# Optimization experiments

Measured on AMD Instinct MI355X. Metric: run time of the kernel, lower is better.

## Reference

```python
import jax, jax.numpy as jnp
import numpy as np

N = 50000
HID = 128
NH = 4
E_RES, E_SEQ, E_KNN = 100000, 100000, 200000
BN_EPS = 1e-5
NEG_SLOPE = 0.2


def _gat(h, src, dst, W, al, ar, resW, b):
    """DGL-style GATConv (eval mode: feat_drop off, residual=True, bias).
    h: (N, in), W/resW: (in, H*out), al/ar: (H, out), b: (H*out,)"""
    Hh, out = al.shape
    feat = (h @ W).reshape(N, Hh, out)                 # (N, H, out)
    el = jnp.sum(feat * al, axis=-1)                   # (N, H)
    er = jnp.sum(feat * ar, axis=-1)                   # (N, H)
    e = jax.nn.leaky_relu(el[src] + er[dst], NEG_SLOPE)  # (E, H)
    # edge softmax over incoming edges of each dst node (numerically stable)
    m = jax.ops.segment_max(e, dst, num_segments=N)    # (N, H)
    ex = jnp.exp(e - m[dst])
    s = jax.ops.segment_sum(ex, dst, num_segments=N)
    a = ex / s[dst]                                    # (E, H)
    msg = a[:, :, None] * feat[src]                    # (E, H, out)
    rst = jax.ops.segment_sum(msg, dst, num_segments=N)  # (N, H, out)
    return rst + (h @ resW).reshape(N, Hh, out) + b.reshape(1, Hh, out)


def _hetero(h, src_res, dst_res, src_seq, dst_seq, src_knn, dst_knn, W, al, ar, resW, b):
    # HeteroGraphConv with aggregate='sum' over relations, then mean over heads
    r = _gat(h, src_res, dst_res, W[0], al[0], ar[0], resW[0], b[0])
    r = r + _gat(h, src_seq, dst_seq, W[1], al[1], ar[1], resW[1], b[1])
    r = r + _gat(h, src_knn, dst_knn, W[2], al[2], ar[2], resW[2], b[2])
    return jnp.mean(r, axis=1)                         # (N, out)


def setup_inputs() -> dict:
    key = jax.random.key(0)
    ks = iter(jax.random.split(key, 32))
    inp = {}
    inp["x"] = jax.random.normal(next(ks), (N, HID), jnp.float32)
    inp["src_res"] = jax.random.randint(next(ks), (E_RES,), 0, N, jnp.int32)
    inp["dst_res"] = jax.random.randint(next(ks), (E_RES,), 0, N, jnp.int32)
    inp["src_seq"] = jax.random.randint(next(ks), (E_SEQ,), 0, N, jnp.int32)
    inp["dst_seq"] = jax.random.randint(next(ks), (E_SEQ,), 0, N, jnp.int32)
    inp["src_knn"] = jax.random.randint(next(ks), (E_KNN,), 0, N, jnp.int32)
    inp["dst_knn"] = jax.random.randint(next(ks), (E_KNN,), 0, N, jnp.int32)
    sc = 0.05
    for l in (0, 1):
        inp[f"W{l}"] = jax.random.normal(next(ks), (3, HID, NH * HID), jnp.float32) * sc
        inp[f"al{l}"] = jax.random.normal(next(ks), (3, NH, HID), jnp.float32) * sc
        inp[f"ar{l}"] = jax.random.normal(next(ks), (3, NH, HID), jnp.float32) * sc
        inp[f"resW{l}"] = jax.random.normal(next(ks), (3, HID, NH * HID), jnp.float32) * sc
        inp[f"b{l}"] = jax.random.normal(next(ks), (3, NH * HID), jnp.float32) * sc
    inp["fc_W"] = jax.random.normal(next(ks), (HID, HID), jnp.float32) * sc
    inp["fc_b"] = jax.random.normal(next(ks), (HID,), jnp.float32) * sc
    inp["bn_gamma"] = jnp.ones((HID,), jnp.float32)
    inp["bn_beta"] = jnp.zeros((HID,), jnp.float32)
    inp["bn_mean"] = jax.random.normal(next(ks), (HID,), jnp.float32) * sc
    inp["bn_var"] = jax.random.uniform(next(ks), (HID,), jnp.float32)
    return inp


def reference(x, src_res, dst_res, src_seq, dst_seq, src_knn, dst_knn,
              W0, al0, ar0, resW0, b0, W1, al1, ar1, resW1, b1,
              fc_W, fc_b, bn_gamma, bn_beta, bn_mean, bn_var):
    # layer 0: hetero GAT, head-mean, fc + ReLU + BatchNorm (eval), dropout=identity
    h = _hetero(x, src_res, dst_res, src_seq, dst_seq, src_knn, dst_knn,
                W0, al0, ar0, resW0, b0)
    h = jax.nn.relu(h @ fc_W + fc_b)
    h = (h - bn_mean) / jnp.sqrt(bn_var + BN_EPS) * bn_gamma + bn_beta
    # layer 1 (final): hetero GAT, head-mean
    out = _hetero(h, src_res, dst_res, src_seq, dst_seq, src_knn, dst_knn,
                  W1, al1, ar1, resW1, b1)
    return out
```

## Files before the change

kernel.cpp:

```cpp
#include <hip/hip_runtime.h>
#include <hip/hip_bf16.h>
#include <math.h>
#include <stdint.h>

#define NNODES 50000
#define SCHUNK 4096
#define AW 1664
#define XOFF 1536

typedef __bf16 bf16x8 __attribute__((ext_vector_type(8)));
typedef float f32x4 __attribute__((ext_vector_type(4)));
typedef unsigned short u16;
typedef unsigned int u32;

__device__ __forceinline__ float lrelu(float x){ return x >= 0.f ? x : 0.2f*x; }
__device__ __forceinline__ float b2f(u16 u){ union{ u32 i; float f; } c; c.i = ((u32)u)<<16; return c.f; }
__device__ __forceinline__ float lo2f(u32 v){ union{ u32 i; float f; } c; c.i = v<<16; return c.f; }
__device__ __forceinline__ float hi2f(u32 v){ union{ u32 i; float f; } c; c.i = v & 0xffff0000u; return c.f; }
__device__ __forceinline__ u16 f2b(float f){ __hip_bfloat16 h = __float2bfloat16(f); return *(u16*)&h; }
__device__ __forceinline__ u32 packbf(float a, float b){ return (u32)f2b(a) | ((u32)f2b(b) << 16); }

#define GLDS16(g, l) __builtin_amdgcn_global_load_lds( \
    (const __attribute__((address_space(1))) void*)(g), \
    (__attribute__((address_space(3))) void*)(l), 16, 0, 0)

__global__ void prep_b(const float* __restrict__ W0, const float* __restrict__ W1,
                       const float* __restrict__ resW0, const float* __restrict__ resW1,
                       const float* __restrict__ b0, const float* __restrict__ b1,
                       u16* __restrict__ Btb, float* __restrict__ biasf)
{
    int gid = blockIdx.x*blockDim.x + threadIdx.x;
    if (gid < 2*128*AW){
        int l = gid / (128*AW);
        int rem = gid - l*(128*AW);
        int c = rem / AW;
        int j = rem - c*AW;
        const float* W  = l ? W1 : W0;
        const float* rw = l ? resW1 : resW0;
        float v;
        if (j < XOFF){
            int r = j >> 9, h = (j >> 7) & 3, k = j & 127;
            v = 0.25f * W[(size_t)r*65536 + (size_t)k*512 + h*128 + c];
        } else {
            int k = j - XOFF;
            float s = 0.f;
            for (int r = 0; r < 3; ++r)
                for (int h = 0; h < 4; ++h)
                    s += rw[(size_t)r*65536 + (size_t)k*512 + h*128 + c];
            v = 0.25f * s;
        }
        Btb[gid] = f2b(v);
    }
    if (gid < 256){
        int l = gid >> 7, c = gid & 127;
        const float* bb = l ? b1 : b0;
        float s = 0.f;
        for (int r = 0; r < 3; ++r)
            for (int h = 0; h < 4; ++h)
                s += bb[r*512 + h*128 + c];
        biasf[gid] = 0.25f*s;
    }
}

__global__ void prep_wl(const float* __restrict__ W0, const float* __restrict__ W1,
                        const float* __restrict__ al0, const float* __restrict__ ar0,
                        const float* __restrict__ al1, const float* __restrict__ ar1,
                        const float* __restrict__ fcW,
                        u16* __restrict__ wlb, u16* __restrict__ fcWtb)
{
    int gid = blockIdx.x*blockDim.x + threadIdx.x;
    if (gid < 2*128*128){
        int l = gid >> 14;
        int col = (gid >> 7) & 127;
        int k = gid & 127;
        float v = 0.f;
        if (col < 24){
            int r = col >> 3, lr = (col >> 2) & 1, h = col & 3;
            const float* W = l ? W1 : W0;
            const float* av = l ? (lr ? ar1 : al1) : (lr ? ar0 : al0);
            const float* wrow = W + (size_t)r*65536 + (size_t)k*512 + h*128;
            const float* arow = av + r*512 + h*128;
            for (int cc = 0; cc < 128; ++cc) v += wrow[cc]*arow[cc];
        }
        wlb[gid] = f2b(v);
    }
    if (gid < 128*128){
        int k = gid & 127, n = gid >> 7;
        fcWtb[gid] = f2b(fcW[k*128 + n]);
    }
}

__global__ __launch_bounds__(256) void xprep_kernel(const float* __restrict__ x,
    u16* __restrict__ Ax, const u16* __restrict__ wl, float* __restrict__ el, int M)
{
    __shared__ u16 Xs[64*136];
    __shared__ u16 Ws[32*136];
    const int tid = threadIdx.x;
    const int row0 = blockIdx.x*64;
    #pragma unroll
    for (int p = 0; p < 2; ++p){
        int idx = tid + p*256;
        int c = idx >> 4, kc = (idx & 15)*8;
        float4 v = make_float4(0.f,0.f,0.f,0.f);
        if (c < 24) v = *(const float4*)(wl + c*128 + kc);
        *(float4*)&Ws[c*136 + kc] = v;
    }
    int r = tid >> 2, cq = (tid & 3)*32;
    int grow = row0 + r;
    if (grow < M){
        #pragma unroll
        for (int i = 0; i < 8; ++i){
            float4 v = *(const float4*)(x + (size_t)grow*128 + cq + i*4);
            ushort4 o;
            o.x = f2b(v.x); o.y = f2b(v.y); o.z = f2b(v.z); o.w = f2b(v.w);
            *(ushort4*)(Ax + (size_t)grow*AW + cq + i*4) = o;
            *(ushort4*)&Xs[r*136 + cq + i*4] = o;
        }
    } else {
        ushort4 z; z.x=0; z.y=0; z.z=0; z.w=0;
        #pragma unroll
        for (int i = 0; i < 8; ++i) *(ushort4*)&Xs[r*136 + cq + i*4] = z;
    }
    __syncthreads();
    const int lane = tid & 63, wave = tid >> 6;
    const int r16 = lane & 15, quad = lane >> 4;
    f32x4 acc0 = {}, acc1 = {};
    #pragma unroll
    for (int ks = 0; ks < 4; ++ks){
        int ko = ks*32 + quad*8;
        bf16x8 a  = *(const bf16x8*)&Xs[(wave*16 + r16)*136 + ko];
        bf16x8 b0 = *(const bf16x8*)&Ws[r16*136 + ko];
        bf16x8 b1 = *(const bf16x8*)&Ws[(16 + r16)*136 + ko];
        acc0 = __builtin_amdgcn_mfma_f32_16x16x32_bf16(a, b0, acc0, 0,0,0);
        acc1 = __builtin_amdgcn_mfma_f32_16x16x32_bf16(a, b1, acc1, 0,0,0);
    }
    #pragma unroll
    for (int p = 0; p < 4; ++p){
        int row = row0 + wave*16 + quad*4 + p;
        if (row < M){
            el[(size_t)row*32 + r16] = acc0[p];
            if (r16 < 8) el[(size_t)row*32 + 16 + r16] = acc1[p];
        }
    }
}

__global__ void hist_all(const int* __restrict__ d0, const int* __restrict__ d1,
                         const int* __restrict__ d2, int e0, int e1, int e2,
                         int* __restrict__ cnt)
{
    int g = blockIdx.x*blockDim.x + threadIdx.x;
    if (g >= e0 + e1 + e2) return;
    int rel, idx;
    if (g < e0){ rel = 0; idx = g; }
    else if (g < e0 + e1){ rel = 1; idx = g - e0; }
    else { rel = 2; idx = g - e0 - e1; }
    const int* d = rel == 0 ? d0 : (rel == 1 ? d1 : d2);
    atomicAdd(cnt + (size_t)rel*NNODES + d[idx], 1);
}

__global__ __launch_bounds__(256) void scan_part(const int* __restrict__ cnt_all,
                                                 int* __restrict__ partials, int Nn, int nblk)
{
    int rel = blockIdx.y, blk = blockIdx.x;
    const int* cnt = cnt_all + (size_t)rel*Nn;
    int tid = threadIdx.x;
    int i0 = blk*SCHUNK + tid*16;
    int s = 0;
    #pragma unroll
    for (int k = 0; k < 4; ++k){
        int idx = i0 + k*4;
        if (idx + 3 < Nn){ int4 v = *(const int4*)(cnt + idx); s += v.x+v.y+v.z+v.w; }
        else { for (int j = 0; j < 4; ++j) if (idx+j < Nn) s += cnt[idx+j]; }
    }
    #pragma unroll
    for (int off = 1; off < 64; off <<= 1) s += __shfl_xor(s, off);
    __shared__ int ws[4];
    if ((tid & 63) == 0) ws[tid>>6] = s;
    __syncthreads();
    if (tid == 0) partials[rel*nblk + blk] = ws[0]+ws[1]+ws[2]+ws[3];
}

__global__ __launch_bounds__(256) void scan_write(const int* __restrict__ cnt_all,
                                                  const int* __restrict__ partials,
                                                  int* __restrict__ rp_all, int* __restrict__ cur_all,
                                                  int Nn, int nblk)
{
    int rel = blockIdx.y, blk = blockIdx.x;
    const int* cnt = cnt_all + (size_t)rel*Nn;
    int* rp  = rp_all  + (size_t)rel*(Nn+1);
    int* cur = cur_all + (size_t)rel*Nn;
    int tid = threadIdx.x;
    __shared__ int sOff;
    __shared__ int wsum[4];
    if (tid == 0){
        int o = 0;
        for (int b = 0; b < blk; ++b) o += partials[rel*nblk + b];
        sOff = o;
        if (blk == 0){
            int t = 0;
            for (int b = 0; b < nblk; ++b) t += partials[rel*nblk + b];
            rp[Nn] = t;
        }
    }
    int i0 = blk*SCHUNK + tid*16;
    int v[16];
    int s = 0;
    #pragma unroll
    for (int k = 0; k < 16; ++k){
        int idx = i0 + k;
        v[k] = (idx < Nn) ? cnt[idx] : 0;
        s += v[k];
    }
    int lane = tid & 63;
    int incl = s;
    #pragma unroll
    for (int off = 1; off < 64; off <<= 1){
        int t = __shfl_up(incl, off);
        if (lane >= off) incl += t;
    }
    if (lane == 63) wsum[tid>>6] = incl;
    __syncthreads();
    int woff = 0;
    for (int w = 0; w < (tid>>6); ++w) woff += wsum[w];
    int ex = sOff + woff + incl - s;
    #pragma unroll
    for (int k = 0; k < 16; ++k){
        int idx = i0 + k;
        if (idx < Nn){ rp[idx] = ex; cur[idx] = ex; }
        ex += v[k];
    }
}

__global__ void scatter_all(const int* __restrict__ s0, const int* __restrict__ s1,
                            const int* __restrict__ s2,
                            const int* __restrict__ d0, const int* __restrict__ d1,
                            const int* __restrict__ d2, int e0, int e1, int e2,
                            int* __restrict__ cur, int* __restrict__ colb,
                            int* __restrict__ dste)
{
    int g = blockIdx.x*blockDim.x + threadIdx.x;
    if (g >= e0 + e1 + e2) return;
    int rel, idx, coff;
    if (g < e0){ rel = 0; idx = g; coff = 0; }
    else if (g < e0 + e1){ rel = 1; idx = g - e0; coff = e0; }
    else { rel = 2; idx = g - e0 - e1; coff = e0 + e1; }
    const int* sp = rel == 0 ? s0 : (rel == 1 ? s1 : s2);
    const int* dp = rel == 0 ? d0 : (rel == 1 ? d1 : d2);
    int d = dp[idx];
    int pos = atomicAdd(cur + (size_t)rel*NNODES + d, 1);
    colb[coff + pos] = sp[idx];
    dste[coff + pos] = d;
}

__global__ void wprep(const int* __restrict__ colb, const int* __restrict__ dste,
                      int e0, int e01, int etot,
                      const float* __restrict__ el_all, uint4* __restrict__ rec)
{
    int j = blockIdx.x*blockDim.x + threadIdx.x;
    if (j >= etot) return;
    int rel = (j < e0) ? 0 : ((j < e01) ? 1 : 2);
    int src = colb[j], dst = dste[j];
    float4 es = *(const float4*)(el_all + (size_t)src*32 + rel*8);
    float4 ed = *(const float4*)(el_all + (size_t)dst*32 + rel*8 + 4);
    uint4 o;
    o.x = (u32)src;
    o.y = packbf(__expf(lrelu(es.x + ed.x)), __expf(lrelu(es.y + ed.y)));
    o.z = packbf(__expf(lrelu(es.z + ed.z)), __expf(lrelu(es.w + ed.w)));
    o.w = 0;
    rec[j] = o;
}

__global__ __launch_bounds__(256) void agg3(const int* __restrict__ rowp_all,
    const uint4* __restrict__ rec_all, int e0, int e01,
    const u16* __restrict__ Ax, u16* __restrict__ Abuf, int Nn)
{
    const int rel = blockIdx.y;
    const int tid = threadIdx.x;
    const int o = tid & 15;
    const int n = (blockIdx.x*256 + tid) >> 4;
    if (n >= Nn) return;
    const int* rowp = rowp_all + (size_t)rel*(Nn+1);
    const int coff = (rel == 0) ? 0 : ((rel == 1) ? e0 : e01);
    const uint4* rec = rec_all + coff;
    u16* op = Abuf + (size_t)n*AW + rel*512 + o*8;

    int beg = rowp[n], end = rowp[n+1];
    if (beg >= end){
        uint4 z; z.x = 0; z.y = 0; z.z = 0; z.w = 0;
        #pragma unroll
        for (int h = 0; h < 4; ++h) *(uint4*)(op + h*128) = z;
        return;
    }
    float acc[4][8] = {};
    float us0 = 0.f, us1 = 0.f, us2 = 0.f, us3 = 0.f;

    uint4 ra = rec[beg];
    uint4 xa = *(const uint4*)(Ax + (size_t)ra.x*AW + o*8);
    uint4 rb = ra, xb = xa;
    if (beg + 1 < end){
        rb = rec[beg+1];
        xb = *(const uint4*)(Ax + (size_t)rb.x*AW + o*8);
    }
    for (int j = beg; j < end; ++j){
        uint4 rc = rb, xc = xb;
        if (j + 2 < end){
            rc = rec[j+2];
            xc = *(const uint4*)(Ax + (size_t)rc.x*AW + o*8);
        }
        float w0 = lo2f(ra.y), w1 = hi2f(ra.y), w2 = lo2f(ra.z), w3 = hi2f(ra.z);
        us0 += w0; us1 += w1; us2 += w2; us3 += w3;
        float xv[8];
        xv[0] = lo2f(xa.x); xv[1] = hi2f(xa.x);
        xv[2] = lo2f(xa.y); xv[3] = hi2f(xa.y);
        xv[4] = lo2f(xa.z); xv[5] = hi2f(xa.z);
        xv[6] = lo2f(xa.w); xv[7] = hi2f(xa.w);
        #pragma unroll
        for (int c = 0; c < 8; ++c){
            acc[0][c] = fmaf(w0, xv[c], acc[0][c]);
            acc[1][c] = fmaf(w1, xv[c], acc[1][c]);
            acc[2][c] = fmaf(w2, xv[c], acc[2][c]);
            acc[3][c] = fmaf(w3, xv[c], acc[3][c]);
        }
        ra = rb; xa = xb; rb = rc; xb = xc;
    }
    float inv[4] = {1.f/us0, 1.f/us1, 1.f/us2, 1.f/us3};
    #pragma unroll
    for (int h = 0; h < 4; ++h){
        uint4 ov;
        ov.x = packbf(acc[h][0]*inv[h], acc[h][1]*inv[h]);
        ov.y = packbf(acc[h][2]*inv[h], acc[h][3]*inv[h]);
        ov.z = packbf(acc[h][4]*inv[h], acc[h][5]*inv[h]);
        ov.w = packbf(acc[h][6]*inv[h], acc[h][7]*inv[h]);
        *(uint4*)(op + h*128) = ov;
    }
}

template<int EPI, int ELR>
__global__ __launch_bounds__(256) void gemm_f(
    const u16* __restrict__ A, int Astride, int K,
    const u16* __restrict__ Bt,
    float* __restrict__ Cf, u16* __restrict__ Cb, int Cstride, int M,
    const float* __restrict__ bias, const float* __restrict__ gamma,
    const float* __restrict__ beta, const float* __restrict__ mean,
    const float* __restrict__ var,
    const u16* __restrict__ wl, float* __restrict__ el)
{
    __shared__ u16 smem[24576];
    const int tid = threadIdx.x;
    const int row0 = blockIdx.x*64;
    const int lane = tid & 63, wave = tid >> 6;
    const int wm = (wave >> 1)*32, wn = (wave & 1)*64;
    const int r16 = lane & 15, quad = lane >> 4;
    const int swzbase = r16 & 7;
    f32x4 acc[2][4] = {};

    const int r8 = lane >> 3, jc = lane & 7;
    const int soff = ((jc ^ r8) << 3);
    int gA0 = row0 + wave*16 + r8;      if (gA0 >= M) gA0 = M - 1;
    int gA1 = row0 + wave*16 + 8 + r8;  if (gA1 >= M) gA1 = M - 1;
    const u16* srcA0 = A + (size_t)gA0*Astride + soff;
    const u16* srcA1 = A + (size_t)gA1*Astride + soff;
    const u16* srcB0 = Bt + (size_t)(wave*32      + r8)*K + soff;
    const u16* srcB1 = Bt + (size_t)(wave*32 + 8  + r8)*K + soff;
    const u16* srcB2 = Bt + (size_t)(wave*32 + 16 + r8)*K + soff;
    const u16* srcB3 = Bt + (size_t)(wave*32 + 24 + r8)*K + soff;
    const int nk = K >> 6;

    #define STAGE(buf, k0) do { \
        u16* As_ = smem + (buf)*12288; \
        u16* Bs_ = As_ + 4096; \
        GLDS16(srcA0 + (k0), As_ + wave*1024); \
        GLDS16(srcA1 + (k0), As_ + wave*1024 + 512); \
        GLDS16(srcB0 + (k0), Bs_ + wave*2048); \
        GLDS16(srcB1 + (k0), Bs_ + wave*2048 + 512); \
        GLDS16(srcB2 + (k0), Bs_ + wave*2048 + 1024); \
        GLDS16(srcB3 + (k0), Bs_ + wave*2048 + 1536); \
    } while (0)

    STAGE(0, 0);
    __syncthreads();
    for (int t = 0; t < nk; ++t){
        int cur = t & 1;
        if (t + 1 < nk) STAGE(cur ^ 1, (t + 1) << 6);
        const u16* As = smem + cur*12288;
        const u16* Bs = As + 4096;
        #pragma unroll
        for (int ks = 0; ks < 2; ++ks){
            int swz = ((ks*4 + quad) ^ swzbase) << 3;
            bf16x8 a0 = *(const bf16x8*)&As[(wm + r16)*64 + swz];
            bf16x8 a1 = *(const bf16x8*)&As[(wm + 16 + r16)*64 + swz];
            #pragma unroll
            for (int j = 0; j < 4; ++j){
                bf16x8 b = *(const bf16x8*)&Bs[(wn + j*16 + r16)*64 + swz];
                acc[0][j] = __builtin_amdgcn_mfma_f32_16x16x32_bf16(a0, b, acc[0][j], 0,0,0);
                acc[1][j] = __builtin_amdgcn_mfma_f32_16x16x32_bf16(a1, b, acc[1][j], 0,0,0);
            }
        }
        __syncthreads();
    }
    #undef STAGE

    u16* Cs = smem;
    u16* Ws = smem + 64*136;
    if (ELR){
        #pragma unroll
        for (int p = 0; p < 2; ++p){
            int idx = tid + p*256;
            int c = idx >> 4, kc = (idx & 15)*8;
            float4 v = make_float4(0.f,0.f,0.f,0.f);
            if (c < 24) v = *(const float4*)(wl + c*128 + kc);
            *(float4*)&Ws[c*136 + kc] = v;
        }
    }
    #pragma unroll
    for (int i = 0; i < 2; ++i){
        #pragma unroll
        for (int p = 0; p < 4; ++p){
            int rl = wm + i*16 + quad*4 + p;
            int row = row0 + rl;
            #pragma unroll
            for (int j = 0; j < 4; ++j){
                int col = wn + j*16 + r16;
                float v = acc[i][j][p] + bias[col];
                if (EPI == 2){
                    float t = fmaxf(v, 0.f);
                    v = (t - mean[col]) * rsqrtf(var[col] + 1e-5f) * gamma[col] + beta[col];
                }
                u16 vb = f2b(v);
                if (row < M){
                    if (EPI == 1) Cf[(size_t)row*Cstride + col] = v;
                    else          Cb[(size_t)row*Cstride + col] = vb;
                }
                if (ELR) Cs[rl*136 + col] = vb;
            }
        }
    }
    if (ELR){
        __syncthreads();
        f32x4 e0 = {}, e1 = {};
        #pragma unroll
        for (int ks = 0; ks < 4; ++ks){
            int ko = ks*32 + quad*8;
            bf16x8 a  = *(const bf16x8*)&Cs[(wave*16 + r16)*136 + ko];
            bf16x8 b0 = *(const bf16x8*)&Ws[r16*136 + ko];
            bf16x8 b1 = *(const bf16x8*)&Ws[(16 + r16)*136 + ko];
            e0 = __builtin_amdgcn_mfma_f32_16x16x32_bf16(a, b0, e0, 0,0,0);
            e1 = __builtin_amdgcn_mfma_f32_16x16x32_bf16(a, b1, e1, 0,0,0);
        }
        #pragma unroll
        for (int p = 0; p < 4; ++p){
            int row = row0 + wave*16 + quad*4 + p;
            if (row < M){
                el[(size_t)row*32 + r16] = e0[p];
                if (r16 < 8) el[(size_t)row*32 + 16 + r16] = e1[p];
            }
        }
    }
}

static inline char* align256(char* p){ return (char*)(((uintptr_t)p + 255) & ~(uintptr_t)255); }

extern "C" void kernel_launch(void* const* d_in, const int* in_sizes, int n_in,
                              void* d_out, int out_size, void* d_ws, size_t ws_size,
                              hipStream_t stream)
{
    const float* x      = (const float*)d_in[0];
    const int* srcs[3]  = {(const int*)d_in[1], (const int*)d_in[3], (const int*)d_in[5]};
    const int* dsts[3]  = {(const int*)d_in[2], (const int*)d_in[4], (const int*)d_in[6]};
    const int  E[3]     = {in_sizes[1], in_sizes[3], in_sizes[5]};
    const float* W0     = (const float*)d_in[7];
    const float* al0    = (const float*)d_in[8];
    const float* ar0    = (const float*)d_in[9];
    const float* resW0  = (const float*)d_in[10];
    const float* b0     = (const float*)d_in[11];
    const float* W1     = (const float*)d_in[12];
    const float* al1    = (const float*)d_in[13];
    const float* ar1    = (const float*)d_in[14];
    const float* resW1  = (const float*)d_in[15];
    const float* b1     = (const float*)d_in[16];
    const float* fcW    = (const float*)d_in[17];
    const float* fcb    = (const float*)d_in[18];
    const float* gamma  = (const float*)d_in[19];
    const float* beta   = (const float*)d_in[20];
    const float* bmean  = (const float*)d_in[21];
    const float* bvar   = (const float*)d_in[22];
    float* out = (float*)d_out;

    char* p = (char*)d_ws;
    u16*   Abuf  = (u16*)p;   p += (size_t)NNODES*AW*2;    p = align256(p);
    float* el    = (float*)p; p += (size_t)NNODES*32*4;    p = align256(p);
    u16*   hmb   = (u16*)p;   p += (size_t)NNODES*128*2;   p = align256(p);
    int*   cnt   = (int*)p;   p += (size_t)3*NNODES*4;     p = align256(p);
    int*   rowp  = (int*)p;   p += (size_t)3*(NNODES+1)*4; p = align256(p);
    int*   cur   = (int*)p;   p += (size_t)3*NNODES*4;     p = align256(p);
    int*   colb  = (int*)p;   p += (size_t)(E[0]+E[1]+E[2])*4; p = align256(p);
    int*   dste  = (int*)p;   p += (size_t)(E[0]+E[1]+E[2])*4; p = align256(p);
    uint4* rec   = (uint4*)p; p += (size_t)(E[0]+E[1]+E[2])*16; p = align256(p);
    u16*   Btb   = (u16*)p;   p += (size_t)2*128*AW*2;     p = align256(p);
    u16*   wlb   = (u16*)p;   p += (size_t)2*128*128*2;    p = align256(p);
    u16*   fcWtb = (u16*)p;   p += (size_t)128*128*2;      p = align256(p);
    float* biasf = (float*)p; p += (size_t)2*128*4;        p = align256(p);
    int*   parts = (int*)p;   p += (size_t)3*64*4;

    const int NBLK = (NNODES + SCHUNK - 1)/SCHUNK;
    const int MB = (NNODES + 63)/64;
    const int AGGBLKS = (NNODES*16 + 255)/256;
    const int ETOT = E[0] + E[1] + E[2];
    dim3 blk(256);
    u16* Ax = Abuf + XOFF;

    hipMemsetAsync(cnt, 0, (size_t)3*NNODES*sizeof(int), stream);
    prep_b <<<(2*128*AW + 255)/256, blk, 0, stream>>>(W0, W1, resW0, resW1, b0, b1, Btb, biasf);
    prep_wl<<<(2*128*128 + 255)/256, blk, 0, stream>>>(W0, W1, al0, ar0, al1, ar1, fcW, wlb, fcWtb);
    xprep_kernel<<<MB, blk, 0, stream>>>(x, Ax, wlb, el, NNODES);
    hist_all<<<(ETOT + 255)/256, blk, 0, stream>>>(dsts[0], dsts[1], dsts[2], E[0], E[1], E[2], cnt);
    scan_part <<<dim3(NBLK,3), blk, 0, stream>>>(cnt, parts, NNODES, NBLK);
    scan_write<<<dim3(NBLK,3), blk, 0, stream>>>(cnt, parts, rowp, cur, NNODES, NBLK);
    scatter_all<<<(ETOT + 255)/256, blk, 0, stream>>>(srcs[0], srcs[1], srcs[2],
                                                      dsts[0], dsts[1], dsts[2],
                                                      E[0], E[1], E[2], cur, colb, dste);

    wprep<<<(ETOT + 255)/256, blk, 0, stream>>>(colb, dste, E[0], E[0]+E[1], ETOT, el, rec);
    agg3<<<dim3(AGGBLKS,3), blk, 0, stream>>>(rowp, rec, E[0], E[0]+E[1], Ax, Abuf, NNODES);
    gemm_f<4,0><<<MB, blk, 0, stream>>>(Abuf, AW, AW, Btb, nullptr, hmb, 128, NNODES,
                                        biasf, nullptr, nullptr, nullptr, nullptr, nullptr, nullptr);
    gemm_f<2,1><<<MB, blk, 0, stream>>>(hmb, 128, 128, fcWtb, nullptr, Ax, AW, NNODES,
                                        fcb, gamma, beta, bmean, bvar, wlb + 16384, el);

    wprep<<<(ETOT + 255)/256, blk, 0, stream>>>(colb, dste, E[0], E[0]+E[1], ETOT, el, rec);
    agg3<<<dim3(AGGBLKS,3), blk, 0, stream>>>(rowp, rec, E[0], E[0]+E[1], Ax, Abuf, NNODES);
    gemm_f<1,0><<<MB, blk, 0, stream>>>(Abuf, AW, AW, Btb + (size_t)128*AW, out, nullptr, 128, NNODES,
                                        biasf + 128, nullptr, nullptr, nullptr, nullptr, nullptr, nullptr);
}
```

Before: 390.0 us.

## Fuse edge aggregation with projection GEMM to drop wide intermediate buffer

Replaces the separate aggregation kernel and the wide 1664-column GEMM with one fused kernel. Each wave aggregates neighbor features for 16 rows per relation in registers, packs them directly into MFMA A-fragments, and multiplies against B tiles streamed into LDS with double buffering. The residual term comes from a compact 128-wide X buffer. This removes the write and re-read of the large Abuf intermediate. In exchange it uses heavy register pressure (128 floats of accumulators plus 16 fragments), per-block syncs, and serialises edge aggregation with the MFMA work, giving lower gather parallelism (one lane group per row instead of 16 threads per row per relation).

```diff
diff --git a/kernel.cpp b/kernel.cpp
--- a/kernel.cpp
+++ b/kernel.cpp
@@ -14,7 +14,6 @@
 typedef unsigned int u32;
 
 __device__ __forceinline__ float lrelu(float x){ return x >= 0.f ? x : 0.2f*x; }
-__device__ __forceinline__ float b2f(u16 u){ union{ u32 i; float f; } c; c.i = ((u32)u)<<16; return c.f; }
 __device__ __forceinline__ float lo2f(u32 v){ union{ u32 i; float f; } c; c.i = v<<16; return c.f; }
 __device__ __forceinline__ float hi2f(u32 v){ union{ u32 i; float f; } c; c.i = v & 0xffff0000u; return c.f; }
 __device__ __forceinline__ u16 f2b(float f){ __hip_bfloat16 h = __float2bfloat16(f); return *(u16*)&h; }
@@ -49,7 +48,7 @@
                     s += rw[(size_t)r*65536 + (size_t)k*512 + h*128 + c];
             v = 0.25f * s;
         }
-        Btb[gid] = f2b(v);
+        Btb[(size_t)l*128*AW + (size_t)(j>>3)*1024 + c*8 + (j&7)] = f2b(v);
     }
     if (gid < 256){
         int l = gid >> 7, c = gid & 127;
@@ -91,7 +90,7 @@
 }
 
 __global__ __launch_bounds__(256) void xprep_kernel(const float* __restrict__ x,
-    u16* __restrict__ Ax, const u16* __restrict__ wl, float* __restrict__ el, int M)
+    u16* __restrict__ Xg, const u16* __restrict__ wl, float* __restrict__ el, int M)
 {
     __shared__ u16 Xs[64*136];
     __shared__ u16 Ws[32*136];
@@ -113,7 +112,7 @@
             float4 v = *(const float4*)(x + (size_t)grow*128 + cq + i*4);
             ushort4 o;
             o.x = f2b(v.x); o.y = f2b(v.y); o.z = f2b(v.z); o.w = f2b(v.w);
-            *(ushort4*)(Ax + (size_t)grow*AW + cq + i*4) = o;
+            *(ushort4*)(Xg + (size_t)grow*128 + cq + i*4) = o;
             *(ushort4*)&Xs[r*136 + cq + i*4] = o;
         }
     } else {
@@ -270,68 +269,138 @@
     rec[j] = o;
 }
 
-__global__ __launch_bounds__(256) void agg3(const int* __restrict__ rowp_all,
-    const uint4* __restrict__ rec_all, int e0, int e01,
-    const u16* __restrict__ Ax, u16* __restrict__ Abuf, int Nn)
-{
-    const int rel = blockIdx.y;
+template<int EPI>
+__global__ __launch_bounds__(256, 2) void fused_gat(
+    const int* __restrict__ rowp_all, const uint4* __restrict__ rec_all,
+    int e0, int e01,
+    const u16* __restrict__ Xg, const u16* __restrict__ Btg,
+    float* __restrict__ Cf, u16* __restrict__ Cb, int M,
+    const float* __restrict__ bias)
+{
+    __shared__ u16 smem[8192];
     const int tid = threadIdx.x;
-    const int o = tid & 15;
-    const int n = (blockIdx.x*256 + tid) >> 4;
-    if (n >= Nn) return;
-    const int* rowp = rowp_all + (size_t)rel*(Nn+1);
-    const int coff = (rel == 0) ? 0 : ((rel == 1) ? e0 : e01);
-    const uint4* rec = rec_all + coff;
-    u16* op = Abuf + (size_t)n*AW + rel*512 + o*8;
-
-    int beg = rowp[n], end = rowp[n+1];
-    if (beg >= end){
-        uint4 z; z.x = 0; z.y = 0; z.z = 0; z.w = 0;
-        #pragma unroll
-        for (int h = 0; h < 4; ++h) *(uint4*)(op + h*128) = z;
-        return;
-    }
-    float acc[4][8] = {};
-    float us0 = 0.f, us1 = 0.f, us2 = 0.f, us3 = 0.f;
-
-    uint4 ra = rec[beg];
-    uint4 xa = *(const uint4*)(Ax + (size_t)ra.x*AW + o*8);
-    uint4 rb = ra, xb = xa;
-    if (beg + 1 < end){
-        rb = rec[beg+1];
-        xb = *(const uint4*)(Ax + (size_t)rb.x*AW + o*8);
-    }
-    for (int j = beg; j < end; ++j){
-        uint4 rc = rb, xc = xb;
-        if (j + 2 < end){
-            rc = rec[j+2];
-            xc = *(const uint4*)(Ax + (size_t)rc.x*AW + o*8);
-        }
-        float w0 = lo2f(ra.y), w1 = hi2f(ra.y), w2 = lo2f(ra.z), w3 = hi2f(ra.z);
-        us0 += w0; us1 += w1; us2 += w2; us3 += w3;
-        float xv[8];
-        xv[0] = lo2f(xa.x); xv[1] = hi2f(xa.x);
-        xv[2] = lo2f(xa.y); xv[3] = hi2f(xa.y);
-        xv[4] = lo2f(xa.z); xv[5] = hi2f(xa.z);
-        xv[6] = lo2f(xa.w); xv[7] = hi2f(xa.w);
-        #pragma unroll
-        for (int c = 0; c < 8; ++c){
-            acc[0][c] = fmaf(w0, xv[c], acc[0][c]);
-            acc[1][c] = fmaf(w1, xv[c], acc[1][c]);
-            acc[2][c] = fmaf(w2, xv[c], acc[2][c]);
-            acc[3][c] = fmaf(w3, xv[c], acc[3][c]);
-        }
-        ra = rb; xa = xb; rb = rc; xb = xc;
-    }
-    float inv[4] = {1.f/us0, 1.f/us1, 1.f/us2, 1.f/us3};
-    #pragma unroll
-    for (int h = 0; h < 4; ++h){
-        uint4 ov;
-        ov.x = packbf(acc[h][0]*inv[h], acc[h][1]*inv[h]);
-        ov.y = packbf(acc[h][2]*inv[h], acc[h][3]*inv[h]);
-        ov.z = packbf(acc[h][4]*inv[h], acc[h][5]*inv[h]);
-        ov.w = packbf(acc[h][6]*inv[h], acc[h][7]*inv[h]);
-        *(uint4*)(op + h*128) = ov;
+    const int lane = tid & 63, wave = tid >> 6;
+    const int r16 = lane & 15, quad = lane >> 4;
+    const int row0 = blockIdx.x*64;
+    const int nd = row0 + wave*16 + r16;
+
+    f32x4 cacc[8] = {};
+    bf16x8 afrag[16];
+
+    #define STAGEB(buf, t) do { \
+        const u16* s0_ = Btg + (size_t)(t)*4096; \
+        GLDS16(s0_ + tid*8,        smem + (buf)*4096 + wave*512); \
+        GLDS16(s0_ + 2048 + tid*8, smem + (buf)*4096 + 2048 + wave*512); \
+    } while(0)
+
+    STAGEB(0, 0);
+
+    for (int r = 0; r < 3; ++r){
+        const int* rp = rowp_all + (size_t)r*(NNODES+1);
+        int beg = 0, end = 0;
+        if (nd < M){ beg = rp[nd]; end = rp[nd+1]; }
+        const int coff = (r == 0) ? 0 : ((r == 1) ? e0 : e01);
+        const uint4* rc = rec_all + coff;
+        float ac[4][4][8] = {};
+        float us0 = 0.f, us1 = 0.f, us2 = 0.f, us3 = 0.f;
+        uint4 ra = {0,0,0,0};
+        uint4 p0 = {0,0,0,0}, p1 = {0,0,0,0}, p2 = {0,0,0,0}, p3 = {0,0,0,0};
+        if (beg < end){
+            ra = rc[beg];
+            const u16* xr = Xg + (size_t)ra.x*128 + quad*8;
+            p0 = *(const uint4*)(xr);      p1 = *(const uint4*)(xr + 32);
+            p2 = *(const uint4*)(xr + 64); p3 = *(const uint4*)(xr + 96);
+        }
+        for (int j = beg; j < end; ++j){
+            uint4 rb = ra, q0 = p0, q1 = p1, q2 = p2, q3 = p3;
+            if (j + 1 < end){
+                rb = rc[j+1];
+                const u16* xr = Xg + (size_t)rb.x*128 + quad*8;
+                q0 = *(const uint4*)(xr);      q1 = *(const uint4*)(xr + 32);
+                q2 = *(const uint4*)(xr + 64); q3 = *(const uint4*)(xr + 96);
+            }
+            float w0 = lo2f(ra.y), w1 = hi2f(ra.y), w2 = lo2f(ra.z), w3 = hi2f(ra.z);
+            us0 += w0; us1 += w1; us2 += w2; us3 += w3;
+            #define PROCM(m, pv) do { \
+                float xv[8]; \
+                xv[0]=lo2f(pv.x); xv[1]=hi2f(pv.x); xv[2]=lo2f(pv.y); xv[3]=hi2f(pv.y); \
+                xv[4]=lo2f(pv.z); xv[5]=hi2f(pv.z); xv[6]=lo2f(pv.w); xv[7]=hi2f(pv.w); \
+                _Pragma("unroll") \
+                for (int c = 0; c < 8; ++c){ \
+                    ac[0][m][c] = fmaf(w0, xv[c], ac[0][m][c]); \
+                    ac[1][m][c] = fmaf(w1, xv[c], ac[1][m][c]); \
+                    ac[2][m][c] = fmaf(w2, xv[c], ac[2][m][c]); \
+                    ac[3][m][c] = fmaf(w3, xv[c], ac[3][m][c]); \
+                } \
+            } while(0)
+            PROCM(0, p0); PROCM(1, p1); PROCM(2, p2); PROCM(3, p3);
+            #undef PROCM
+            ra = rb; p0 = q0; p1 = q1; p2 = q2; p3 = q3;
+        }
+        float ivs[4];
+        ivs[0] = us0 > 0.f ? 1.f/us0 : 0.f;
+        ivs[1] = us1 > 0.f ? 1.f/us1 : 0.f;
+        ivs[2] = us2 > 0.f ? 1.f/us2 : 0.f;
+        ivs[3] = us3 > 0.f ? 1.f/us3 : 0.f;
+        #pragma unroll
+        for (int h = 0; h < 4; ++h){
+            #pragma unroll
+            for (int m = 0; m < 4; ++m){
+                union { bf16x8 v; u32 w[4]; } u;
+                u.w[0] = packbf(ac[h][m][0]*ivs[h], ac[h][m][1]*ivs[h]);
+                u.w[1] = packbf(ac[h][m][2]*ivs[h], ac[h][m][3]*ivs[h]);
+                u.w[2] = packbf(ac[h][m][4]*ivs[h], ac[h][m][5]*ivs[h]);
+                u.w[3] = packbf(ac[h][m][6]*ivs[h], ac[h][m][7]*ivs[h]);
+                afrag[h*4 + m] = u.v;
+            }
+        }
+        if (r == 0) __syncthreads();
+        #pragma unroll
+        for (int m2 = 0; m2 < 16; ++m2){
+            STAGEB((m2+1)&1, r*16 + m2 + 1);
+            const u16* Bs = smem + (m2&1)*4096 + quad*1024;
+            #pragma unroll
+            for (int j = 0; j < 8; ++j){
+                bf16x8 b = *(const bf16x8*)&Bs[(j*16 + r16)*8];
+                cacc[j] = __builtin_amdgcn_mfma_f32_16x16x32_bf16(afrag[m2], b, cacc[j], 0,0,0);
+            }
+            __syncthreads();
+        }
+    }
+    {
+        int xrow = nd < M ? nd : M - 1;
+        const u16* xr = Xg + (size_t)xrow*128 + quad*8;
+        bf16x8 xf0 = *(const bf16x8*)(xr);
+        bf16x8 xf1 = *(const bf16x8*)(xr + 32);
+        bf16x8 xf2 = *(const bf16x8*)(xr + 64);
+        bf16x8 xf3 = *(const bf16x8*)(xr + 96);
+        #pragma unroll
+        for (int m2 = 0; m2 < 4; ++m2){
+            if (m2 < 3) STAGEB((m2+1)&1, 49 + m2);
+            const u16* Bs = smem + (m2&1)*4096 + quad*1024;
+            bf16x8 a = m2 == 0 ? xf0 : (m2 == 1 ? xf1 : (m2 == 2 ? xf2 : xf3));
+            #pragma unroll
+            for (int j = 0; j < 8; ++j){
+                bf16x8 b = *(const bf16x8*)&Bs[(j*16 + r16)*8];
+                cacc[j] = __builtin_amdgcn_mfma_f32_16x16x32_bf16(a, b, cacc[j], 0,0,0);
+            }
+            __syncthreads();
+        }
+    }
+    #undef STAGEB
+    #pragma unroll
+    for (int j = 0; j < 8; ++j){
+        int col = j*16 + r16;
+        float bi = bias[col];
+        #pragma unroll
+        for (int p = 0; p < 4; ++p){
+            int row = row0 + wave*16 + quad*4 + p;
+            if (row < M){
+                float v = cacc[j][p] + bi;
+                if (EPI == 1) Cf[(size_t)row*128 + col] = v;
+                else          Cb[(size_t)row*128 + col] = f2b(v);
+            }
+        }
     }
 }
 
@@ -487,9 +556,10 @@
     float* out = (float*)d_out;
 
     char* p = (char*)d_ws;
-    u16*   Abuf  = (u16*)p;   p += (size_t)NNODES*AW*2;    p = align256(p);
+    u16*   Xg    = (u16*)p;   p += (size_t)NNODES*128*2;   p = align256(p);
+    u16*   hx1   = (u16*)p;   p += (size_t)NNODES*128*2;   p = align256(p);
+    u16*   hmb   = (u16*)p;   p += (size_t)NNODES*128*2;   p = align256(p);
     float* el    = (float*)p; p += (size_t)NNODES*32*4;    p = align256(p);
-    u16*   hmb   = (u16*)p;   p += (size_t)NNODES*128*2;   p = align256(p);
     int*   cnt   = (int*)p;   p += (size_t)3*NNODES*4;     p = align256(p);
     int*   rowp  = (int*)p;   p += (size_t)3*(NNODES+1)*4; p = align256(p);
     int*   cur   = (int*)p;   p += (size_t)3*NNODES*4;     p = align256(p);
@@ -504,15 +574,13 @@
 
     const int NBLK = (NNODES + SCHUNK - 1)/SCHUNK;
     const int MB = (NNODES + 63)/64;
-    const int AGGBLKS = (NNODES*16 + 255)/256;
     const int ETOT = E[0] + E[1] + E[2];
     dim3 blk(256);
-    u16* Ax = Abuf + XOFF;
 
     hipMemsetAsync(cnt, 0, (size_t)3*NNODES*sizeof(int), stream);
     prep_b <<<(2*128*AW + 255)/256, blk, 0, stream>>>(W0, W1, resW0, resW1, b0, b1, Btb, biasf);
     prep_wl<<<(2*128*128 + 255)/256, blk, 0, stream>>>(W0, W1, al0, ar0, al1, ar1, fcW, wlb, fcWtb);
-    xprep_kernel<<<MB, blk, 0, stream>>>(x, Ax, wlb, el, NNODES);
+    xprep_kernel<<<MB, blk, 0, stream>>>(x, Xg, wlb, el, NNODES);
     hist_all<<<(ETOT + 255)/256, blk, 0, stream>>>(dsts[0], dsts[1], dsts[2], E[0], E[1], E[2], cnt);
     scan_part <<<dim3(NBLK,3), blk, 0, stream>>>(cnt, parts, NNODES, NBLK);
     scan_write<<<dim3(NBLK,3), blk, 0, stream>>>(cnt, parts, rowp, cur, NNODES, NBLK);
@@ -521,14 +589,12 @@
                                                       E[0], E[1], E[2], cur, colb, dste);
 
     wprep<<<(ETOT + 255)/256, blk, 0, stream>>>(colb, dste, E[0], E[0]+E[1], ETOT, el, rec);
-    agg3<<<dim3(AGGBLKS,3), blk, 0, stream>>>(rowp, rec, E[0], E[0]+E[1], Ax, Abuf, NNODES);
-    gemm_f<4,0><<<MB, blk, 0, stream>>>(Abuf, AW, AW, Btb, nullptr, hmb, 128, NNODES,
-                                        biasf, nullptr, nullptr, nullptr, nullptr, nullptr, nullptr);
-    gemm_f<2,1><<<MB, blk, 0, stream>>>(hmb, 128, 128, fcWtb, nullptr, Ax, AW, NNODES,
+    fused_gat<4><<<MB, blk, 0, stream>>>(rowp, rec, E[0], E[0]+E[1], Xg, Btb,
+                                         nullptr, hmb, NNODES, biasf);
+    gemm_f<2,1><<<MB, blk, 0, stream>>>(hmb, 128, 128, fcWtb, nullptr, hx1, 128, NNODES,
                                         fcb, gamma, beta, bmean, bvar, wlb + 16384, el);
 
     wprep<<<(ETOT + 255)/256, blk, 0, stream>>>(colb, dste, E[0], E[0]+E[1], ETOT, el, rec);
-    agg3<<<dim3(AGGBLKS,3), blk, 0, stream>>>(rowp, rec, E[0], E[0]+E[1], Ax, Abuf, NNODES);
-    gemm_f<1,0><<<MB, blk, 0, stream>>>(Abuf, AW, AW, Btb + (size_t)128*AW, out, nullptr, 128, NNODES,
-                                        biasf + 128, nullptr, nullptr, nullptr, nullptr, nullptr, nullptr);
-}
+    fused_gat<1><<<MB, blk, 0, stream>>>(rowp, rec, E[0], E[0]+E[1], hx1, Btb + (size_t)128*AW,
+                                         out, nullptr, NNODES, biasf + 128);
+}
```

Result: no change. 396.3 us (+1.6%).
